# Optimization experiments

Hardware: AMD Instinct MI355X
Metric: run time of the kernel (lower is better)

## Reference

```python
import jax, jax.numpy as jnp
import numpy as np

DIM = 1024
N_HEADS = 16
B, T = 2, 2048


def setup_inputs() -> dict:
    key = jax.random.key(0)
    ks = jax.random.split(key, 9)
    s = 1.0 / np.sqrt(DIM)
    return {
        "x": jax.random.normal(ks[0], (B, T, DIM), dtype=jnp.float32),
        "Wq": jax.random.normal(ks[1], (DIM, DIM), dtype=jnp.float32) * s,
        "bq": jnp.zeros((DIM,), dtype=jnp.float32),
        "Wk": jax.random.normal(ks[2], (DIM, DIM), dtype=jnp.float32) * s,
        "bk": jnp.zeros((DIM,), dtype=jnp.float32),
        "Wv": jax.random.normal(ks[3], (DIM, DIM), dtype=jnp.float32) * s,
        "bv": jnp.zeros((DIM,), dtype=jnp.float32),
        "Wo": jax.random.normal(ks[4], (DIM, DIM), dtype=jnp.float32) * s,
        "bo": jnp.zeros((DIM,), dtype=jnp.float32),
    }


def reference(x, Wq, bq, Wk, bk, Wv, bv, Wo, bo):
    Bv, Tv, d = x.shape
    n = N_HEADS
    hd = d // n
    # projections (torch Linear: x @ W.T + b)
    Q = x @ Wq.T + bq
    K = x @ Wk.T + bk
    V = x @ Wv.T + bv
    # [B, n, T, hd]
    Q = Q.reshape(Bv, Tv, n, hd).transpose(0, 2, 1, 3)
    K = K.reshape(Bv, Tv, n, hd).transpose(0, 2, 1, 3)
    V = V.reshape(Bv, Tv, n, hd).transpose(0, 2, 1, 3)
    # NOTE: original scales by full model dim, not head dim
    scale = 1.0 / jnp.sqrt(jnp.asarray(d, dtype=x.dtype))
    scores = jnp.einsum('bnqd,bnkd->bnqk', Q, K) * scale
    causal = jnp.tril(jnp.ones((Tv, Tv), dtype=bool))
    scores = jnp.where(causal, scores, jnp.asarray(-jnp.inf, dtype=scores.dtype))
    attn = jax.nn.softmax(scores, axis=-1)
    out = jnp.einsum('bnqk,bnkd->bnqd', attn, V)
    out = out.transpose(0, 2, 1, 3).reshape(Bv, Tv, d)
    return out @ Wo.T + bo
```

## Files before the change

### kernel.cpp

```cpp
#include <hip/hip_runtime.h>
#include <math.h>

#define DIMN 1024
#define NH 16
#define HD 64
#define BATCH 2
#define SEQ 2048
#define MROWS (BATCH*SEQ)

typedef unsigned short u16;
typedef unsigned int u32;
typedef __attribute__((ext_vector_type(8))) short bf16x8;
typedef __attribute__((ext_vector_type(4))) float f32x4;

__device__ __forceinline__ u16 f2bf(float f) {
    unsigned u = __float_as_uint(f);
    u += 0x7FFF + ((u >> 16) & 1);
    return (u16)(u >> 16);
}
__device__ __forceinline__ float bf2f(u16 s) {
    return __uint_as_float(((unsigned)s) << 16);
}

#define GLOADLDS16(g, s)                                                     \
    __builtin_amdgcn_global_load_lds(                                        \
        (const __attribute__((address_space(1))) void*)(g),                  \
        (__attribute__((address_space(3))) void*)(s), 16, 0, 0)

__global__ __launch_bounds__(256)
void split_hilo(const float* __restrict__ src, u16* __restrict__ h,
                u16* __restrict__ l, int n4)
{
    int i = blockIdx.x * 256 + threadIdx.x;
    if (i >= n4) return;
    float4 v = ((const float4*)src)[i];
    ushort4 hv, lv;
    hv.x = f2bf(v.x); lv.x = f2bf(v.x - bf2f(hv.x));
    hv.y = f2bf(v.y); lv.y = f2bf(v.y - bf2f(hv.y));
    hv.z = f2bf(v.z); lv.z = f2bf(v.z - bf2f(hv.z));
    hv.w = f2bf(v.w); lv.w = f2bf(v.w - bf2f(hv.w));
    ((ushort4*)h)[i] = hv;
    ((ushort4*)l)[i] = lv;
}

#define BM 128
#define BN 128
#define BK 32

template<bool QKV>
__global__ __launch_bounds__(256)
void mfma_gemm(const u16* __restrict__ Ah, const u16* __restrict__ Al,
               const u16* __restrict__ Wh0, const u16* __restrict__ Wl0,
               const u16* __restrict__ Wh1, const u16* __restrict__ Wl1,
               const u16* __restrict__ Wh2, const u16* __restrict__ Wl2,
               const float* __restrict__ b0, const float* __restrict__ b1,
               const float* __restrict__ b2,
               u16* __restrict__ Qh, u16* __restrict__ Ql,
               u16* __restrict__ Kh, u16* __restrict__ Kl,
               float* __restrict__ Vw, float* __restrict__ Yout)
{
    __shared__ u16 AhS[BM*BK], AlS[BM*BK], WhS[BN*BK], WlS[BN*BK];

    const u16* Wh = Wh0; const u16* Wl = Wl0; const float* bias = b0;
    if (QKV) {
        if (blockIdx.z == 1)      { Wh = Wh1; Wl = Wl1; bias = b1; }
        else if (blockIdx.z == 2) { Wh = Wh2; Wl = Wl2; bias = b2; }
    }

    const int tid  = threadIdx.x;
    const int lane = tid & 63;
    const int wid  = tid >> 6;
    const int wr   = wid >> 1;
    const int wc   = wid & 1;

    const int m0 = blockIdx.y * BM;
    const int n0 = blockIdx.x * BN;

    const int srow = lane >> 2;
    const int skc  = (lane & 3) << 3;
    const int c0 = wid * 2, c1 = wid * 2 + 1;
    const size_t aoffg0 = (size_t)(m0 + c0*16 + srow) * DIMN + skc;
    const size_t aoffg1 = (size_t)(m0 + c1*16 + srow) * DIMN + skc;
    const size_t woffg0 = (size_t)(n0 + c0*16 + srow) * DIMN + skc;
    const size_t woffg1 = (size_t)(n0 + c1*16 + srow) * DIMN + skc;

    f32x4 acc[4][4];
    #pragma unroll
    for (int m = 0; m < 4; ++m)
        #pragma unroll
        for (int n = 0; n < 4; ++n)
            acc[m][n] = (f32x4){0.f, 0.f, 0.f, 0.f};

    const int fr = lane & 15;
    const int fq = lane >> 4;
    const int aoff = (wr*64 + fr) * BK + fq*8;
    const int boff = (wc*64 + fr) * BK + fq*8;

    for (int k0 = 0; k0 < DIMN; k0 += BK) {
        GLOADLDS16(Ah + aoffg0 + k0, &AhS[c0*512]);
        GLOADLDS16(Ah + aoffg1 + k0, &AhS[c1*512]);
        GLOADLDS16(Al + aoffg0 + k0, &AlS[c0*512]);
        GLOADLDS16(Al + aoffg1 + k0, &AlS[c1*512]);
        GLOADLDS16(Wh + woffg0 + k0, &WhS[c0*512]);
        GLOADLDS16(Wh + woffg1 + k0, &WhS[c1*512]);
        GLOADLDS16(Wl + woffg0 + k0, &WlS[c0*512]);
        GLOADLDS16(Wl + woffg1 + k0, &WlS[c1*512]);
        __syncthreads();

        bf16x8 ah[4], al[4], bh[4], bl[4];
        #pragma unroll
        for (int m = 0; m < 4; ++m) {
            ah[m] = *(const bf16x8*)&AhS[aoff + m*16*BK];
            al[m] = *(const bf16x8*)&AlS[aoff + m*16*BK];
        }
        #pragma unroll
        for (int n = 0; n < 4; ++n) {
            bh[n] = *(const bf16x8*)&WhS[boff + n*16*BK];
            bl[n] = *(const bf16x8*)&WlS[boff + n*16*BK];
        }
        #pragma unroll
        for (int m = 0; m < 4; ++m)
            #pragma unroll
            for (int n = 0; n < 4; ++n) {
                acc[m][n] = __builtin_amdgcn_mfma_f32_16x16x32_bf16(ah[m], bh[n], acc[m][n], 0, 0, 0);
                acc[m][n] = __builtin_amdgcn_mfma_f32_16x16x32_bf16(ah[m], bl[n], acc[m][n], 0, 0, 0);
                acc[m][n] = __builtin_amdgcn_mfma_f32_16x16x32_bf16(al[m], bh[n], acc[m][n], 0, 0, 0);
            }
        __syncthreads();
    }

    #pragma unroll
    for (int n = 0; n < 4; ++n) {
        const int col = n0 + wc*64 + n*16 + fr;
        const float bv = bias[col];
        #pragma unroll
        for (int m = 0; m < 4; ++m) {
            #pragma unroll
            for (int j = 0; j < 4; ++j) {
                const int row = m0 + wr*64 + m*16 + fq*4 + j;
                float v = acc[m][n][j] + bv;
                if (QKV) {
                    const int b_ = row >> 11, t = row & (SEQ - 1);
                    const int hh = col >> 6, d = col & 63;
                    const size_t rb = (((size_t)b_*NH + hh)*SEQ + t)*HD;
                    if (blockIdx.z == 0) {
                        v *= 0.03125f;
                        u16 hv = f2bf(v), lv = f2bf(v - bf2f(hv));
                        Qh[rb + d] = hv; Ql[rb + d] = lv;
                    } else if (blockIdx.z == 1) {
                        u16 hv = f2bf(v), lv = f2bf(v - bf2f(hv));
                        const int ds = d ^ ((t & 7) << 3);
                        Kh[rb + ds] = hv; Kl[rb + ds] = lv;
                    } else {
                        Vw[rb + d] = v;
                    }
                } else {
                    Yout[(size_t)row*DIMN + col] = v;
                }
            }
        }
    }
}

__global__ __launch_bounds__(256)
void convV(const float* __restrict__ Vw, u16* __restrict__ Vth, u16* __restrict__ Vtl)
{
    __shared__ float Vs[64][68];
    const int tid = threadIdx.x;
    const int bh = blockIdx.y;
    const int t0 = blockIdx.x * 64;
    const float* src = Vw + ((size_t)bh*SEQ + t0)*HD;
    #pragma unroll
    for (int k = 0; k < 4; ++k) {
        int f4 = tid + k*256;
        int r = f4 >> 4, c4 = (f4 & 15) << 2;
        *(float4*)&Vs[r][c4] = *(const float4*)(src + (size_t)r*HD + c4);
    }
    __syncthreads();
    const int d  = tid >> 2;
    const int q2 = (tid & 3) << 4;
    u16* oh = Vth + ((size_t)bh*HD + d)*SEQ + t0;
    u16* ol = Vtl + ((size_t)bh*HD + d)*SEQ + t0;
    #pragma unroll
    for (int p = 0; p < 4; ++p) {
        const int lt = q2 + p*4;
        const int t_sw = (lt & 32) | ((((lt >> 3) & 3) ^ (d & 3)) << 3) | (lt & 7);
        ushort4 hv, lv; float v;
        v = Vs[lt + 0][d]; hv.x = f2bf(v); lv.x = f2bf(v - bf2f(hv.x));
        v = Vs[lt + 1][d]; hv.y = f2bf(v); lv.y = f2bf(v - bf2f(hv.y));
        v = Vs[lt + 2][d]; hv.z = f2bf(v); lv.z = f2bf(v - bf2f(hv.z));
        v = Vs[lt + 3][d]; hv.w = f2bf(v); lv.w = f2bf(v - bf2f(hv.w));
        *(ushort4*)(oh + t_sw) = hv;
        *(ushort4*)(ol + t_sw) = lv;
    }
}

__global__ __launch_bounds__(256)
void attn_mfma(const u16* __restrict__ Qhg, const u16* __restrict__ Qlg,
               const u16* __restrict__ Khg, const u16* __restrict__ Klg,
               const u16* __restrict__ Vthg, const u16* __restrict__ Vtlg,
               u16* __restrict__ AH, u16* __restrict__ AL)
{
    __shared__ u16 KVS[2][4][2048];
    __shared__ u16 PhS[4][640];
    __shared__ u16 PlS[4][640];

    const int tid  = threadIdx.x;
    const int lane = tid & 63;
    const int w    = tid >> 6;
    const int fr   = lane & 15;
    const int fq   = lane >> 4;
    const int bh   = blockIdx.y;
    const int b_   = bh >> 4;
    const int h    = bh & 15;

    auto stage = [&](int buf, int kt2) {
        u16* dst = &KVS[buf][w][0];
        if (w < 2) {
            const u16* g = (w == 0 ? Khg : Klg) +
                ((size_t)bh*SEQ + (size_t)kt2*32 + (lane>>3))*HD + ((lane&7)<<3);
            #pragma unroll
            for (int i = 0; i < 4; ++i)
                GLOADLDS16(g + (size_t)i*8*HD, dst + i*512);
        } else {
            const u16* g = (w == 2 ? Vthg : Vtlg) +
                ((size_t)bh*HD + (lane>>2))*SEQ + (size_t)kt2*32 + ((lane&3)<<3);
            #pragma unroll
            for (int i = 0; i < 4; ++i)
                GLOADLDS16(g + (size_t)i*16*SEQ, dst + i*512);
        }
    };

    #pragma unroll 1
    for (int pass = 0; pass < 2; ++pass) {
        const int qt   = pass ? (31 - blockIdx.x) : blockIdx.x;
        const int qabs = qt*64 + w*16 + fr;
        const int nt   = 2*qt + 2;

        bf16x8 qh[2], ql[2];
        {
            const size_t qrow = ((size_t)bh*SEQ + qabs)*HD;
            #pragma unroll
            for (int ks = 0; ks < 2; ++ks) {
                qh[ks] = *(const bf16x8*)&Qhg[qrow + ks*32 + (fq<<3)];
                ql[ks] = *(const bf16x8*)&Qlg[qrow + ks*32 + (fq<<3)];
            }
        }

        f32x4 o[4];
        #pragma unroll
        for (int md = 0; md < 4; ++md) o[md] = (f32x4){0.f,0.f,0.f,0.f};
        float mrun = -INFINITY, lrun = 0.f;

        __syncthreads();
        stage(0, 0);
        int cur = 0;

        for (int kt = 0; kt < nt; ++kt) {
            __syncthreads();
            if (kt + 1 < nt) stage(cur ^ 1, kt + 1);

            f32x4 s0 = (f32x4){0.f,0.f,0.f,0.f};
            f32x4 s1 = (f32x4){0.f,0.f,0.f,0.f};
            #pragma unroll
            for (int ks = 0; ks < 2; ++ks) {
                const int sl = (((ks*4 + fq) ^ (fr & 7)) << 3);
                bf16x8 a0h = *(const bf16x8*)&KVS[cur][0][fr*64 + sl];
                bf16x8 a0l = *(const bf16x8*)&KVS[cur][1][fr*64 + sl];
                bf16x8 a1h = *(const bf16x8*)&KVS[cur][0][(16+fr)*64 + sl];
                bf16x8 a1l = *(const bf16x8*)&KVS[cur][1][(16+fr)*64 + sl];
                s0 = __builtin_amdgcn_mfma_f32_16x16x32_bf16(a0h, qh[ks], s0, 0,0,0);
                s0 = __builtin_amdgcn_mfma_f32_16x16x32_bf16(a0h, ql[ks], s0, 0,0,0);
                s0 = __builtin_amdgcn_mfma_f32_16x16x32_bf16(a0l, qh[ks], s0, 0,0,0);
                s1 = __builtin_amdgcn_mfma_f32_16x16x32_bf16(a1h, qh[ks], s1, 0,0,0);
                s1 = __builtin_amdgcn_mfma_f32_16x16x32_bf16(a1h, ql[ks], s1, 0,0,0);
                s1 = __builtin_amdgcn_mfma_f32_16x16x32_bf16(a1l, qh[ks], s1, 0,0,0);
            }

            const int kb = kt*32 + fq*4;
            #pragma unroll
            for (int j = 0; j < 4; ++j) {
                if (kb + j      > qabs) s0[j] = -INFINITY;
                if (kb + 16 + j > qabs) s1[j] = -INFINITY;
            }

            float pm = fmaxf(fmaxf(fmaxf(s0[0],s0[1]), fmaxf(s0[2],s0[3])),
                             fmaxf(fmaxf(s1[0],s1[1]), fmaxf(s1[2],s1[3])));
            pm = fmaxf(pm, __shfl_xor(pm, 16));
            pm = fmaxf(pm, __shfl_xor(pm, 32));
            const float mnew = fmaxf(mrun, pm);
            const float fac  = __expf(mrun - mnew);
            float p[8];
            #pragma unroll
            for (int j = 0; j < 4; ++j) {
                p[j]   = __expf(s0[j] - mnew);
                p[4+j] = __expf(s1[j] - mnew);
            }
            float ls = ((p[0]+p[1]) + (p[2]+p[3])) + ((p[4]+p[5]) + (p[6]+p[7]));
            ls += __shfl_xor(ls, 16);
            ls += __shfl_xor(ls, 32);
            lrun = lrun * fac + ls;
            mrun = mnew;
            #pragma unroll
            for (int md = 0; md < 4; ++md) {
                o[md][0] *= fac; o[md][1] *= fac; o[md][2] *= fac; o[md][3] *= fac;
            }

            u16 ph[8], pl[8];
            #pragma unroll
            for (int i = 0; i < 8; ++i) {
                ph[i] = f2bf(p[i]);
                pl[i] = f2bf(p[i] - bf2f(ph[i]));
            }
            {
                const int pb = fr*40 + fq*4;
                uint2 w0, w1;
                w0.x = (u32)ph[0] | ((u32)ph[1] << 16);
                w0.y = (u32)ph[2] | ((u32)ph[3] << 16);
                w1.x = (u32)ph[4] | ((u32)ph[5] << 16);
                w1.y = (u32)ph[6] | ((u32)ph[7] << 16);
                *(uint2*)&PhS[w][pb]      = w0;
                *(uint2*)&PhS[w][pb + 16] = w1;
                w0.x = (u32)pl[0] | ((u32)pl[1] << 16);
                w0.y = (u32)pl[2] | ((u32)pl[3] << 16);
                w1.x = (u32)pl[4] | ((u32)pl[5] << 16);
                w1.y = (u32)pl[6] | ((u32)pl[7] << 16);
                *(uint2*)&PlS[w][pb]      = w0;
                *(uint2*)&PlS[w][pb + 16] = w1;
            }

            bf16x8 bph = *(const bf16x8*)&PhS[w][fr*40 + (fq<<3)];
            bf16x8 bpl = *(const bf16x8*)&PlS[w][fr*40 + (fq<<3)];
            #pragma unroll
            for (int md = 0; md < 4; ++md) {
                const int vsl = ((fq ^ (fr & 3)) << 3);
                bf16x8 avh = *(const bf16x8*)&KVS[cur][2][(md*16+fr)*32 + vsl];
                bf16x8 avl = *(const bf16x8*)&KVS[cur][3][(md*16+fr)*32 + vsl];
                o[md] = __builtin_amdgcn_mfma_f32_16x16x32_bf16(avh, bph, o[md], 0,0,0);
                o[md] = __builtin_amdgcn_mfma_f32_16x16x32_bf16(avh, bpl, o[md], 0,0,0);
                o[md] = __builtin_amdgcn_mfma_f32_16x16x32_bf16(avl, bph, o[md], 0,0,0);
            }
            cur ^= 1;
        }

        const float inv = 1.f / lrun;
        const size_t ob = ((size_t)b_*SEQ + qabs)*DIMN + h*64;
        #pragma unroll
        for (int md = 0; md < 4; ++md) {
            #pragma unroll
            for (int pr = 0; pr < 2; ++pr) {
                const int d0 = md*16 + fq*4 + pr*2;
                const float v0 = o[md][pr*2]   * inv;
                const float v1 = o[md][pr*2+1] * inv;
                u16 h0 = f2bf(v0), l0 = f2bf(v0 - bf2f(h0));
                u16 h1 = f2bf(v1), l1 = f2bf(v1 - bf2f(h1));
                *(u32*)&AH[ob + d0] = (u32)h0 | ((u32)h1 << 16);
                *(u32*)&AL[ob + d0] = (u32)l0 | ((u32)l1 << 16);
            }
        }
    }
}

extern "C" void kernel_launch(void* const* d_in, const int* in_sizes, int n_in,
                              void* d_out, int out_size, void* d_ws, size_t ws_size,
                              hipStream_t stream)
{
    const float* x  = (const float*)d_in[0];
    const float* Wq = (const float*)d_in[1];
    const float* bq = (const float*)d_in[2];
    const float* Wk = (const float*)d_in[3];
    const float* bk = (const float*)d_in[4];
    const float* Wv = (const float*)d_in[5];
    const float* bv = (const float*)d_in[6];
    const float* Wo = (const float*)d_in[7];
    const float* bo = (const float*)d_in[8];
    float* out = (float*)d_out;

    const size_t NX = (size_t)MROWS * DIMN;
    const size_t NW = (size_t)DIMN * DIMN;

    u16* Xh  = (u16*)d_ws;
    u16* Xl  = Xh  + NX;
    u16* WhQ = Xl  + NX;
    u16* WlQ = WhQ + NW;
    u16* WhK = WlQ + NW;
    u16* WlK = WhK + NW;
    u16* WhV = WlK + NW;
    u16* WlV = WhV + NW;
    u16* WhO = WlV + NW;
    u16* WlO = WhO + NW;
    u16* Qh  = WlO + NW;
    u16* Ql  = Qh + NX;
    u16* Kh  = Ql + NX;
    u16* Kl  = Kh + NX;
    u16* Vth = Kl + NX;
    u16* Vtl = Vth + NX;
    float* Vw = (float*)(Vtl + NX);
    u16* AH = Xh;
    u16* AL = Xl;

    const int n4x = (int)(NX / 4);
    const int n4w = (int)(NW / 4);
    split_hilo<<<n4x/256, 256, 0, stream>>>(x,  Xh,  Xl,  n4x);
    split_hilo<<<n4w/256, 256, 0, stream>>>(Wq, WhQ, WlQ, n4w);
    split_hilo<<<n4w/256, 256, 0, stream>>>(Wk, WhK, WlK, n4w);
    split_hilo<<<n4w/256, 256, 0, stream>>>(Wv, WhV, WlV, n4w);
    split_hilo<<<n4w/256, 256, 0, stream>>>(Wo, WhO, WlO, n4w);

    dim3 gq(DIMN / BN, MROWS / BM, 3);
    mfma_gemm<true><<<gq, 256, 0, stream>>>(Xh, Xl, WhQ, WlQ, WhK, WlK, WhV, WlV,
                                            bq, bk, bv, Qh, Ql, Kh, Kl, Vw, nullptr);

    dim3 gv(SEQ / 64, BATCH * NH);
    convV<<<gv, 256, 0, stream>>>(Vw, Vth, Vtl);

    dim3 ga(16, BATCH * NH);
    attn_mfma<<<ga, 256, 0, stream>>>(Qh, Ql, Kh, Kl, Vth, Vtl, AH, AL);

    dim3 gp(DIMN / BN, MROWS / BM, 1);
    mfma_gemm<false><<<gp, 256, 0, stream>>>(AH, AL, WhO, WlO, nullptr, nullptr,
                                             nullptr, nullptr, bo, nullptr, nullptr,
                                             nullptr, nullptr, nullptr, nullptr,
                                             nullptr, out);
}
```

Before: 380.2 us.

## Batch weight splits, retile output GEMM, add lazy softmax rescale and MFMA priority

The four weight hi/lo split launches become one launch with a z-dimension. The GEMM is templated on N-fragment count so the output projection uses 128x64 tiles, doubling its block count, and the grid axes are swapped so blocks sharing an N tile launch together. In attention, the online softmax skips rescaling the accumulator unless the running max grows by more than a threshold, and MFMA sections are wrapped in s_setprio to raise wave priority. The lazy rescale lets exponentials reach up to e^8 before correction, which slightly changes numerical behaviour.

```diff
diff --git a/kernel.cpp b/kernel.cpp
--- a/kernel.cpp
+++ b/kernel.cpp
@@ -43,11 +43,34 @@
     ((ushort4*)l)[i] = lv;
 }
 
-#define BM 128
-#define BN 128
-#define BK 32
-
-template<bool QKV>
+__global__ __launch_bounds__(256)
+void split4_hilo(const float* __restrict__ s0, const float* __restrict__ s1,
+                 const float* __restrict__ s2, const float* __restrict__ s3,
+                 u16* __restrict__ h0, u16* __restrict__ l0,
+                 u16* __restrict__ h1, u16* __restrict__ l1,
+                 u16* __restrict__ h2, u16* __restrict__ l2,
+                 u16* __restrict__ h3, u16* __restrict__ l3, int n4)
+{
+    const float* src; u16* h; u16* l;
+    switch (blockIdx.z) {
+        case 0: src = s0; h = h0; l = l0; break;
+        case 1: src = s1; h = h1; l = l1; break;
+        case 2: src = s2; h = h2; l = l2; break;
+        default: src = s3; h = h3; l = l3; break;
+    }
+    int i = blockIdx.x * 256 + threadIdx.x;
+    if (i >= n4) return;
+    float4 v = ((const float4*)src)[i];
+    ushort4 hv, lv;
+    hv.x = f2bf(v.x); lv.x = f2bf(v.x - bf2f(hv.x));
+    hv.y = f2bf(v.y); lv.y = f2bf(v.y - bf2f(hv.y));
+    hv.z = f2bf(v.z); lv.z = f2bf(v.z - bf2f(hv.z));
+    hv.w = f2bf(v.w); lv.w = f2bf(v.w - bf2f(hv.w));
+    ((ushort4*)h)[i] = hv;
+    ((ushort4*)l)[i] = lv;
+}
+
+template<int NF, bool QKV>
 __global__ __launch_bounds__(256)
 void mfma_gemm(const u16* __restrict__ Ah, const u16* __restrict__ Al,
                const u16* __restrict__ Wh0, const u16* __restrict__ Wl0,
@@ -59,6 +82,9 @@
                u16* __restrict__ Kh, u16* __restrict__ Kl,
                float* __restrict__ Vw, float* __restrict__ Yout)
 {
+    constexpr int BM = 128;
+    constexpr int BN = NF * 32;
+    constexpr int BK = 32;
     __shared__ u16 AhS[BM*BK], AlS[BM*BK], WhS[BN*BK], WlS[BN*BK];
 
     const u16* Wh = Wh0; const u16* Wl = Wl0; const float* bias = b0;
@@ -73,8 +99,8 @@
     const int wr   = wid >> 1;
     const int wc   = wid & 1;
 
-    const int m0 = blockIdx.y * BM;
-    const int n0 = blockIdx.x * BN;
+    const int m0 = blockIdx.x * BM;
+    const int n0 = blockIdx.y * BN;
 
     const int srow = lane >> 2;
     const int skc  = (lane & 3) << 3;
@@ -83,45 +109,48 @@
     const size_t aoffg1 = (size_t)(m0 + c1*16 + srow) * DIMN + skc;
     const size_t woffg0 = (size_t)(n0 + c0*16 + srow) * DIMN + skc;
     const size_t woffg1 = (size_t)(n0 + c1*16 + srow) * DIMN + skc;
-
-    f32x4 acc[4][4];
+    const bool doW = (c0 < BN/16);
+
+    f32x4 acc[4][NF];
     #pragma unroll
     for (int m = 0; m < 4; ++m)
         #pragma unroll
-        for (int n = 0; n < 4; ++n)
+        for (int n = 0; n < NF; ++n)
             acc[m][n] = (f32x4){0.f, 0.f, 0.f, 0.f};
 
     const int fr = lane & 15;
     const int fq = lane >> 4;
     const int aoff = (wr*64 + fr) * BK + fq*8;
-    const int boff = (wc*64 + fr) * BK + fq*8;
+    const int boff = (wc*(NF*16) + fr) * BK + fq*8;
 
     for (int k0 = 0; k0 < DIMN; k0 += BK) {
         GLOADLDS16(Ah + aoffg0 + k0, &AhS[c0*512]);
         GLOADLDS16(Ah + aoffg1 + k0, &AhS[c1*512]);
         GLOADLDS16(Al + aoffg0 + k0, &AlS[c0*512]);
         GLOADLDS16(Al + aoffg1 + k0, &AlS[c1*512]);
-        GLOADLDS16(Wh + woffg0 + k0, &WhS[c0*512]);
-        GLOADLDS16(Wh + woffg1 + k0, &WhS[c1*512]);
-        GLOADLDS16(Wl + woffg0 + k0, &WlS[c0*512]);
-        GLOADLDS16(Wl + woffg1 + k0, &WlS[c1*512]);
+        if (doW) {
+            GLOADLDS16(Wh + woffg0 + k0, &WhS[c0*512]);
+            GLOADLDS16(Wh + woffg1 + k0, &WhS[c1*512]);
+            GLOADLDS16(Wl + woffg0 + k0, &WlS[c0*512]);
+            GLOADLDS16(Wl + woffg1 + k0, &WlS[c1*512]);
+        }
         __syncthreads();
 
-        bf16x8 ah[4], al[4], bh[4], bl[4];
+        bf16x8 ah[4], al[4], bh[NF], bl[NF];
         #pragma unroll
         for (int m = 0; m < 4; ++m) {
             ah[m] = *(const bf16x8*)&AhS[aoff + m*16*BK];
             al[m] = *(const bf16x8*)&AlS[aoff + m*16*BK];
         }
         #pragma unroll
-        for (int n = 0; n < 4; ++n) {
+        for (int n = 0; n < NF; ++n) {
             bh[n] = *(const bf16x8*)&WhS[boff + n*16*BK];
             bl[n] = *(const bf16x8*)&WlS[boff + n*16*BK];
         }
         #pragma unroll
         for (int m = 0; m < 4; ++m)
             #pragma unroll
-            for (int n = 0; n < 4; ++n) {
+            for (int n = 0; n < NF; ++n) {
                 acc[m][n] = __builtin_amdgcn_mfma_f32_16x16x32_bf16(ah[m], bh[n], acc[m][n], 0, 0, 0);
                 acc[m][n] = __builtin_amdgcn_mfma_f32_16x16x32_bf16(ah[m], bl[n], acc[m][n], 0, 0, 0);
                 acc[m][n] = __builtin_amdgcn_mfma_f32_16x16x32_bf16(al[m], bh[n], acc[m][n], 0, 0, 0);
@@ -130,8 +159,8 @@
     }
 
     #pragma unroll
-    for (int n = 0; n < 4; ++n) {
-        const int col = n0 + wc*64 + n*16 + fr;
+    for (int n = 0; n < NF; ++n) {
+        const int col = n0 + wc*(NF*16) + n*16 + fr;
         const float bv = bias[col];
         #pragma unroll
         for (int m = 0; m < 4; ++m) {
@@ -262,6 +291,7 @@
 
             f32x4 s0 = (f32x4){0.f,0.f,0.f,0.f};
             f32x4 s1 = (f32x4){0.f,0.f,0.f,0.f};
+            __builtin_amdgcn_s_setprio(1);
             #pragma unroll
             for (int ks = 0; ks < 2; ++ks) {
                 const int sl = (((ks*4 + fq) ^ (fr & 7)) << 3);
@@ -276,6 +306,7 @@
                 s1 = __builtin_amdgcn_mfma_f32_16x16x32_bf16(a1h, ql[ks], s1, 0,0,0);
                 s1 = __builtin_amdgcn_mfma_f32_16x16x32_bf16(a1l, qh[ks], s1, 0,0,0);
             }
+            __builtin_amdgcn_s_setprio(0);
 
             const int kb = kt*32 + fq*4;
             #pragma unroll
@@ -288,23 +319,28 @@
                              fmaxf(fmaxf(s1[0],s1[1]), fmaxf(s1[2],s1[3])));
             pm = fmaxf(pm, __shfl_xor(pm, 16));
             pm = fmaxf(pm, __shfl_xor(pm, 32));
-            const float mnew = fmaxf(mrun, pm);
-            const float fac  = __expf(mrun - mnew);
+
+            if (!__all(pm - mrun <= 8.0f)) {
+                const float mnew = fmaxf(mrun, pm);
+                const float fac  = __expf(mrun - mnew);
+                lrun *= fac;
+                #pragma unroll
+                for (int md = 0; md < 4; ++md) {
+                    o[md][0] *= fac; o[md][1] *= fac;
+                    o[md][2] *= fac; o[md][3] *= fac;
+                }
+                mrun = mnew;
+            }
             float p[8];
             #pragma unroll
             for (int j = 0; j < 4; ++j) {
-                p[j]   = __expf(s0[j] - mnew);
-                p[4+j] = __expf(s1[j] - mnew);
+                p[j]   = __expf(s0[j] - mrun);
+                p[4+j] = __expf(s1[j] - mrun);
             }
             float ls = ((p[0]+p[1]) + (p[2]+p[3])) + ((p[4]+p[5]) + (p[6]+p[7]));
             ls += __shfl_xor(ls, 16);
             ls += __shfl_xor(ls, 32);
-            lrun = lrun * fac + ls;
-            mrun = mnew;
-            #pragma unroll
-            for (int md = 0; md < 4; ++md) {
-                o[md][0] *= fac; o[md][1] *= fac; o[md][2] *= fac; o[md][3] *= fac;
-            }
+            lrun += ls;
 
             u16 ph[8], pl[8];
             #pragma unroll
@@ -331,6 +367,7 @@
 
             bf16x8 bph = *(const bf16x8*)&PhS[w][fr*40 + (fq<<3)];
             bf16x8 bpl = *(const bf16x8*)&PlS[w][fr*40 + (fq<<3)];
+            __builtin_amdgcn_s_setprio(1);
             #pragma unroll
             for (int md = 0; md < 4; ++md) {
                 const int vsl = ((fq ^ (fr & 3)) << 3);
@@ -340,6 +377,7 @@
                 o[md] = __builtin_amdgcn_mfma_f32_16x16x32_bf16(avh, bpl, o[md], 0,0,0);
                 o[md] = __builtin_amdgcn_mfma_f32_16x16x32_bf16(avl, bph, o[md], 0,0,0);
             }
+            __builtin_amdgcn_s_setprio(0);
             cur ^= 1;
         }
 
@@ -381,14 +419,10 @@
 
     u16* Xh  = (u16*)d_ws;
     u16* Xl  = Xh  + NX;
-    u16* WhQ = Xl  + NX;
-    u16* WlQ = WhQ + NW;
-    u16* WhK = WlQ + NW;
-    u16* WlK = WhK + NW;
-    u16* WhV = WlK + NW;
-    u16* WlV = WhV + NW;
-    u16* WhO = WlV + NW;
-    u16* WlO = WhO + NW;
+    u16* WhQ = Xl  + NX;  u16* WlQ = WhQ + NW;
+    u16* WhK = WlQ + NW;  u16* WlK = WhK + NW;
+    u16* WhV = WlK + NW;  u16* WlV = WhV + NW;
+    u16* WhO = WlV + NW;  u16* WlO = WhO + NW;
     u16* Qh  = WlO + NW;
     u16* Ql  = Qh + NX;
     u16* Kh  = Ql + NX;
@@ -401,15 +435,14 @@
 
     const int n4x = (int)(NX / 4);
     const int n4w = (int)(NW / 4);
-    split_hilo<<<n4x/256, 256, 0, stream>>>(x,  Xh,  Xl,  n4x);
-    split_hilo<<<n4w/256, 256, 0, stream>>>(Wq, WhQ, WlQ, n4w);
-    split_hilo<<<n4w/256, 256, 0, stream>>>(Wk, WhK, WlK, n4w);
-    split_hilo<<<n4w/256, 256, 0, stream>>>(Wv, WhV, WlV, n4w);
-    split_hilo<<<n4w/256, 256, 0, stream>>>(Wo, WhO, WlO, n4w);
-
-    dim3 gq(DIMN / BN, MROWS / BM, 3);
-    mfma_gemm<true><<<gq, 256, 0, stream>>>(Xh, Xl, WhQ, WlQ, WhK, WlK, WhV, WlV,
-                                            bq, bk, bv, Qh, Ql, Kh, Kl, Vw, nullptr);
+    split_hilo<<<n4x/256, 256, 0, stream>>>(x, Xh, Xl, n4x);
+    dim3 gs(n4w/256, 1, 4);
+    split4_hilo<<<gs, 256, 0, stream>>>(Wq, Wk, Wv, Wo,
+                                        WhQ, WlQ, WhK, WlK, WhV, WlV, WhO, WlO, n4w);
+
+    dim3 gq(MROWS/128, DIMN/128, 3);
+    mfma_gemm<4, true><<<gq, 256, 0, stream>>>(Xh, Xl, WhQ, WlQ, WhK, WlK, WhV, WlV,
+                                               bq, bk, bv, Qh, Ql, Kh, Kl, Vw, nullptr);
 
     dim3 gv(SEQ / 64, BATCH * NH);
     convV<<<gv, 256, 0, stream>>>(Vw, Vth, Vtl);
@@ -417,9 +450,9 @@
     dim3 ga(16, BATCH * NH);
     attn_mfma<<<ga, 256, 0, stream>>>(Qh, Ql, Kh, Kl, Vth, Vtl, AH, AL);
 
-    dim3 gp(DIMN / BN, MROWS / BM, 1);
-    mfma_gemm<false><<<gp, 256, 0, stream>>>(AH, AL, WhO, WlO, nullptr, nullptr,
-                                             nullptr, nullptr, bo, nullptr, nullptr,
-                                             nullptr, nullptr, nullptr, nullptr,
-                                             nullptr, out);
-}
+    dim3 gp(MROWS/128, DIMN/64, 1);
+    mfma_gemm<2, false><<<gp, 256, 0, stream>>>(AH, AL, WhO, WlO, nullptr, nullptr,
+                                                nullptr, nullptr, bo, nullptr, nullptr,
+                                                nullptr, nullptr, nullptr, nullptr,
+                                                nullptr, out);
+}
```

Measured after the change: 339.2 us. 10.8% less time.
